# Optimization experiments

Measured on AMD Instinct MI355X. Metric: run time of the kernel, lower is better.

## Reference

```python
import jax, jax.numpy as jnp
import numpy as np

C_IN, C_OUT, K, DG, PAD = 256, 256, 3, 2, 1
EPS = 1e-5


def setup_inputs() -> dict:
    key = jax.random.key(0)
    k = jax.random.split(key, 8)
    B, H, W = 4, 64, 64
    x = jax.random.normal(k[0], (B, C_IN, H, W), jnp.float32)
    # offset/mask conv (DCNv2 pack): 3 * dg * k * k output channels
    w_off = jax.random.normal(k[1], (3 * DG * K * K, C_IN, K, K), jnp.float32) * 0.01
    b_off = jnp.zeros((3 * DG * K * K,), jnp.float32)
    # main deformable conv weight
    w = jax.random.normal(k[2], (C_OUT, C_IN, K, K), jnp.float32) * (1.0 / np.sqrt(C_IN * K * K))
    b = jnp.zeros((C_OUT,), jnp.float32)
    # BatchNorm (eval mode: running stats)
    gamma = jnp.ones((C_OUT,), jnp.float32)
    beta = jnp.zeros((C_OUT,), jnp.float32)
    running_mean = jax.random.normal(k[3], (C_OUT,), jnp.float32) * 0.1
    running_var = jax.random.uniform(k[4], (C_OUT,), jnp.float32, 0.5, 1.5)
    return dict(x=x, w_off=w_off, b_off=b_off, w=w, b=b, gamma=gamma, beta=beta,
                running_mean=running_mean, running_var=running_var)


def _conv2d_same(x, w, b):
    y = jax.lax.conv_general_dilated(x, w, (1, 1), 'SAME',
                                     dimension_numbers=('NCHW', 'OIHW', 'NCHW'))
    return y + b[None, :, None, None]


def _deform_conv(x, w_off, b_off, w, b):
    B, C, H, W = x.shape
    K2 = K * K
    Cg = C // DG
    # offsets + modulation mask from internal conv (DCNv2 pack)
    om = _conv2d_same(x, w_off, b_off)            # [B, 3*DG*K2, H, W]
    o1, o2, m = jnp.split(om, 3, axis=1)
    mask = jax.nn.sigmoid(m).reshape(B, DG, 1, K2, H * W)
    off_y = o1.reshape(B, DG, K2, H, W)
    off_x = o2.reshape(B, DG, K2, H, W)
    # base sampling grid: output pixel + kernel tap - pad
    ki = jnp.arange(K)
    ky = (jnp.repeat(ki, K) - PAD).astype(jnp.float32)   # [K2]
    kx = (jnp.tile(ki, K) - PAD).astype(jnp.float32)     # [K2]
    py = off_y + ky[:, None, None] + jnp.arange(H, dtype=jnp.float32)[None, :, None]
    px = off_x + kx[:, None, None] + jnp.arange(W, dtype=jnp.float32)[None, None, :]
    y0 = jnp.floor(py)
    x0 = jnp.floor(px)
    ly = (py - y0).reshape(B, DG, 1, K2, H * W)
    lx = (px - x0).reshape(B, DG, 1, K2, H * W)
    y0i = y0.astype(jnp.int32)
    x0i = x0.astype(jnp.int32)
    xg = x.reshape(B, DG, Cg, H * W)

    def gather(yi, xi):
        # zero-padded bilinear corner gather, per deformable group
        valid = (yi >= 0) & (yi < H) & (xi >= 0) & (xi < W)
        lin = jnp.clip(yi, 0, H - 1) * W + jnp.clip(xi, 0, W - 1)
        v = jnp.take_along_axis(xg[:, :, :, None, :],
                                lin.reshape(B, DG, 1, K2, H * W), axis=-1)
        return v * valid.reshape(B, DG, 1, K2, H * W)

    val = (gather(y0i, x0i) * (1 - ly) * (1 - lx)
           + gather(y0i, x0i + 1) * (1 - ly) * lx
           + gather(y0i + 1, x0i) * ly * (1 - lx)
           + gather(y0i + 1, x0i + 1) * ly * lx)
    val = val * mask                               # [B, DG, Cg, K2, H*W]
    wr = w.reshape(C_OUT, DG, Cg, K2)
    out = jnp.einsum('bgckn,ogck->bon', val, wr).reshape(B, C_OUT, H, W)
    return out + b[None, :, None, None]


def reference(x, w_off, b_off, w, b, gamma, beta, running_mean, running_var):
    y = _deform_conv(x, w_off, b_off, w, b)
    inv = gamma / jnp.sqrt(running_var + EPS)
    y = (y - running_mean[None, :, None, None]) * inv[None, :, None, None] + beta[None, :, None, None]
    return jax.nn.relu(y)
```

## Files before the change

### kernel.cpp

```cpp
#include <hip/hip_runtime.h>
#include <math.h>

typedef __bf16 bf16x8 __attribute__((ext_vector_type(8)));
typedef float  f32x4  __attribute__((ext_vector_type(4)));
typedef int    i32x4  __attribute__((ext_vector_type(4)));

#define MFMA16(a, b, c) __builtin_amdgcn_mfma_f32_16x16x32_bf16((a), (b), (c), 0, 0, 0)

#define ATIDX(r, c) ((r) * 128 + (((c) ^ ((r) & 7)) * 8))

__global__ __launch_bounds__(256) void setup_kernel(
    const float* __restrict__ x, const float* __restrict__ w,
    const float* __restrict__ w_off, const float* __restrict__ bconv,
    const float* __restrict__ gamma, const float* __restrict__ beta,
    const float* __restrict__ mean, const float* __restrict__ var,
    __bf16* __restrict__ xT, __bf16* __restrict__ wFragD,
    __bf16* __restrict__ wFragO, float* __restrict__ sc,
    float* __restrict__ sh) {
  __shared__ float xs[64][65];
  int t = threadIdx.x;
  if (blockIdx.x < 1024) {
    int b = blockIdx.x >> 8, y = (blockIdx.x >> 2) & 63, cc = blockIdx.x & 3;
    for (int i = t; i < 4096; i += 256) {
      int cl = i >> 6, xc = i & 63;
      xs[cl][xc] = x[(((size_t)b * 256 + cc * 64 + cl) * 64 + y) * 64 + xc];
    }
    __syncthreads();
    for (int i = t; i < 4096; i += 256) {
      int xc = i >> 6, cl = i & 63;
      xT[(((size_t)b * 64 + y) * 64 + xc) * 256 + cc * 64 + cl] = (__bf16)xs[cl][xc];
    }
    return;
  }
  int i = (blockIdx.x - 1024) * 256 + t;
  if (i < 589824) {
    int j = i & 7, lane = (i >> 3) & 63, ocb = (i >> 9) & 15;
    int kc = (i >> 13) & 3, gk = i >> 15;
    int klocal = (lane >> 4) * 8 + j;
    int oc = ocb * 16 + (lane & 15);
    int c = kc * 32 + klocal;
    int g = gk / 9, ktap = gk % 9;
    wFragD[i] = (__bf16)w[((size_t)oc * 256 + g * 128 + c) * 9 + ktap];
  } else {
    int i2 = i - 589824;
    int j = i2 & 7, lane = (i2 >> 3) & 63, ocb = (i2 >> 9) & 3;
    int kc = (i2 >> 11) & 7, tap = i2 >> 14;
    int klocal = (lane >> 4) * 8 + j;
    int oc = ocb * 16 + (lane & 15);
    int ci = kc * 32 + klocal;
    wFragO[i2] = (oc < 54) ? (__bf16)w_off[((size_t)oc * 256 + ci) * 9 + tap]
                           : (__bf16)0.f;
  }
  if (i < 256) {
    float s = gamma[i] * rsqrtf(var[i] + 1e-5f);
    sc[i] = s;
    sh[i] = (bconv[i] - mean[i]) * s + beta[i];
  }
}

struct PhaseC {
  f32x4 swgtv[18 * 64];
  i32x4 slinv[18 * 64];
  __bf16 atile[2][64 * 128];
};
union FusedLDS {
  __bf16 rowbuf[3 * 66 * 256];
  PhaseC c;
};

__global__ __launch_bounds__(1024) void fused_kernel(
    const __bf16* __restrict__ xT, const __bf16* __restrict__ wFragD,
    const __bf16* __restrict__ wFragO, const float* __restrict__ b_off,
    const float* __restrict__ sc, const float* __restrict__ sh,
    float* __restrict__ out) {
  __shared__ __attribute__((aligned(16))) FusedLDS U;
  __shared__ float omrow[54 * 64];
  int t = threadIdx.x;
  int b = blockIdx.x >> 6, y = blockIdx.x & 63;
  int lane = t & 63, wv = t >> 6;
  int l15 = lane & 15, quad = lane >> 4;
  const __bf16* xTb = xT + (size_t)b * 64 * 64 * 256;
  bf16x8 z8;
  #pragma unroll
  for (int e = 0; e < 8; ++e) z8[e] = (__bf16)0.f;

  for (int i = t; i < 3 * 66 * 32; i += 1024) {
    int c = i & 31, px66 = (i >> 5) % 66, dy = i / 2112;
    int y2 = y + dy - 1, x2 = px66 - 1;
    bf16x8 v = z8;
    if (y2 >= 0 && y2 < 64 && x2 >= 0 && x2 < 64)
      v = *(const bf16x8*)(xTb + ((size_t)y2 * 64 + x2) * 256 + c * 8);
    *(bf16x8*)&U.rowbuf[dy * 16896 + px66 * 256 + ((c ^ (px66 & 7)) * 8)] = v;
  }
  __syncthreads();

  if (wv < 4) {
    int ocq = wv;
    f32x4 acc4[4];
    #pragma unroll
    for (int fm = 0; fm < 4; ++fm) acc4[fm] = (f32x4){0.f, 0.f, 0.f, 0.f};
    for (int tap = 0; tap < 9; ++tap) {
      int dy = tap / 3, dxs = tap % 3;
      const __bf16* bb = wFragO + ((size_t)(tap * 8) * 4 + ocq) * 512 + lane * 8;
      const __bf16* rb = U.rowbuf + dy * 16896;
      #pragma unroll
      for (int kc = 0; kc < 8; ++kc) {
        bf16x8 Bf = *(const bf16x8*)(bb + (size_t)kc * 4 * 512);
        int c = kc * 4 + quad;
        #pragma unroll
        for (int fm = 0; fm < 4; ++fm) {
          int p0 = fm * 16 + l15 + dxs;
          bf16x8 a0 = *(const bf16x8*)&rb[p0 * 256 + ((c ^ (p0 & 7)) * 8)];
          acc4[fm] = MFMA16(a0, Bf, acc4[fm]);
        }
      }
    }
    int oc = ocq * 16 + l15;
    if (oc < 54) {
      float bo = b_off[oc];
      #pragma unroll
      for (int fm = 0; fm < 4; ++fm) {
        f32x4 r = {acc4[fm].x + bo, acc4[fm].y + bo,
                   acc4[fm].z + bo, acc4[fm].w + bo};
        *(f32x4*)&omrow[oc * 64 + fm * 16 + quad * 4] = r;
      }
    }
  }
  __syncthreads();

  for (int i = t; i < 18 * 64; i += 1024) {
    int gk = i >> 6, p = i & 63;
    int k = gk % 9;
    float oy = omrow[gk * 64 + p];
    float ox = omrow[(18 + gk) * 64 + p];
    float mz = omrow[(36 + gk) * 64 + p];
    float mv = 1.f / (1.f + expf(-mz));
    float py  = (float)(y + (k / 3) - 1) + oy;
    float pxf = (float)(p + (k % 3) - 1) + ox;
    float y0f = floorf(py), x0f = floorf(pxf);
    int y0 = (int)y0f, x0 = (int)x0f;
    float ly = py - y0f, lx = pxf - x0f;
    int y1 = y0 + 1, x1 = x0 + 1;
    bool vy0 = (y0 >= 0) && (y0 < 64), vy1 = (y1 >= 0) && (y1 < 64);
    bool vx0 = (x0 >= 0) && (x0 < 64), vx1 = (x1 >= 0) && (x1 < 64);
    int cy0 = min(max(y0, 0), 63), cy1 = min(max(y1, 0), 63);
    int cx0 = min(max(x0, 0), 63), cx1 = min(max(x1, 0), 63);
    f32x4 sv;
    sv.x = (vy0 && vx0) ? (1.f - ly) * (1.f - lx) * mv : 0.f;
    sv.y = (vy0 && vx1) ? (1.f - ly) * lx * mv : 0.f;
    sv.z = (vy1 && vx0) ? ly * (1.f - lx) * mv : 0.f;
    sv.w = (vy1 && vx1) ? ly * lx * mv : 0.f;
    i32x4 lv;
    lv.x = (cy0 * 64 + cx0) * 256;
    lv.y = (cy0 * 64 + cx1) * 256;
    lv.z = (cy1 * 64 + cx0) * 256;
    lv.w = (cy1 * 64 + cx1) * 256;
    U.c.swgtv[i] = sv;
    U.c.slinv[i] = lv;
  }
  __syncthreads();

  {
    int p = t >> 4, c16 = t & 15;
    const __bf16* xg = xTb + c16 * 8;
    f32x4 sv = U.c.swgtv[p];
    i32x4 lv = U.c.slinv[p];
    bf16x8 c0 = *(const bf16x8*)(xg + lv.x);
    bf16x8 c1 = *(const bf16x8*)(xg + lv.y);
    bf16x8 c2 = *(const bf16x8*)(xg + lv.z);
    bf16x8 c3 = *(const bf16x8*)(xg + lv.w);
    bf16x8 o;
    #pragma unroll
    for (int e = 0; e < 8; ++e)
      o[e] = (__bf16)(sv.x * (float)c0[e] + sv.y * (float)c1[e]
                    + sv.z * (float)c2[e] + sv.w * (float)c3[e]);
    *(bf16x8*)&U.c.atile[0][ATIDX(p, c16)] = o;
  }

  f32x4 acc[4][2];
  #pragma unroll
  for (int fm = 0; fm < 4; ++fm) {
    acc[fm][0] = (f32x4){0.f, 0.f, 0.f, 0.f};
    acc[fm][1] = (f32x4){0.f, 0.f, 0.f, 0.f};
  }
  int nq = wv - 8;
  bf16x8 bn0, bn1;
  if (wv >= 8) {
    const __bf16* bb = wFragD + ((size_t)nq * 2) * 512 + lane * 8;
    bn0 = *(const bf16x8*)bb;
    bn1 = *(const bf16x8*)(bb + 512);
  }
  __syncthreads();

  for (int gk = 0; gk < 18; ++gk) {
    if (wv < 8) {
      if (gk < 17) {
        int gn = gk + 1;
        int c16 = t & 15, p = t >> 4;
        const __bf16* xg = xTb + (gn / 9) * 128 + c16 * 8;
        __bf16* dst = U.c.atile[(gk + 1) & 1];
        #pragma unroll
        for (int half = 0; half < 2; ++half) {
          int pp = p + half * 32;
          f32x4 sv = U.c.swgtv[gn * 64 + pp];
          i32x4 lv = U.c.slinv[gn * 64 + pp];
          bf16x8 c0 = *(const bf16x8*)(xg + lv.x);
          bf16x8 c1 = *(const bf16x8*)(xg + lv.y);
          bf16x8 c2 = *(const bf16x8*)(xg + lv.z);
          bf16x8 c3 = *(const bf16x8*)(xg + lv.w);
          bf16x8 o;
          #pragma unroll
          for (int e = 0; e < 8; ++e)
            o[e] = (__bf16)(sv.x * (float)c0[e] + sv.y * (float)c1[e]
                          + sv.z * (float)c2[e] + sv.w * (float)c3[e]);
          *(bf16x8*)&dst[ATIDX(pp, c16)] = o;
        }
      }
    } else {
      const __bf16* at = U.c.atile[gk & 1];
      #pragma unroll
      for (int kc = 0; kc < 4; ++kc) {
        bf16x8 b0 = bn0, b1 = bn1;
        int nidx = gk * 4 + kc + 1;
        if (nidx < 72) {
          const __bf16* bb = wFragD + ((size_t)nidx * 16 + nq * 2) * 512 + lane * 8;
          bn0 = *(const bf16x8*)bb;
          bn1 = *(const bf16x8*)(bb + 512);
        }
        #pragma unroll
        for (int fm = 0; fm < 4; ++fm) {
          bf16x8 a = *(const bf16x8*)&at[ATIDX(fm * 16 + l15, kc * 4 + quad)];
          acc[fm][0] = MFMA16(a, b0, acc[fm][0]);
          acc[fm][1] = MFMA16(a, b1, acc[fm][1]);
        }
      }
    }
    __syncthreads();
  }

  if (wv >= 8) {
    #pragma unroll
    for (int fm = 0; fm < 4; ++fm) {
      #pragma unroll
      for (int fn = 0; fn < 2; ++fn) {
        int oc = nq * 32 + fn * 16 + l15;
        float s = sc[oc], h = sh[oc];
        f32x4 v = acc[fm][fn];
        f32x4 r = {fmaxf(v.x * s + h, 0.f), fmaxf(v.y * s + h, 0.f),
                   fmaxf(v.z * s + h, 0.f), fmaxf(v.w * s + h, 0.f)};
        int pxs = fm * 16 + quad * 4;
        *(f32x4*)(out + (((size_t)b * 256 + oc) * 64 + y) * 64 + pxs) = r;
      }
    }
  }
}

extern "C" void kernel_launch(void* const* d_in, const int* in_sizes, int n_in,
                              void* d_out, int out_size, void* d_ws, size_t ws_size,
                              hipStream_t stream) {
  const float* x     = (const float*)d_in[0];
  const float* w_off = (const float*)d_in[1];
  const float* b_off = (const float*)d_in[2];
  const float* w     = (const float*)d_in[3];
  const float* bconv = (const float*)d_in[4];
  const float* gamma = (const float*)d_in[5];
  const float* beta  = (const float*)d_in[6];
  const float* rmean = (const float*)d_in[7];
  const float* rvar  = (const float*)d_in[8];
  float* out = (float*)d_out;

  __bf16* xT     = (__bf16*)d_ws;
  __bf16* wFragD = (__bf16*)((char*)d_ws + 8388608);
  __bf16* wFragO = (__bf16*)((char*)d_ws + 9568256);
  float*  sc     = (float*)((char*)d_ws + 9863168);
  float*  sh     = (float*)((char*)d_ws + 9864192);

  setup_kernel<<<1024 + 2880, 256, 0, stream>>>(
      x, w, w_off, bconv, gamma, beta, rmean, rvar, xT, wFragD, wFragO, sc, sh);
  fused_kernel<<<4 * 64, 1024, 0, stream>>>(xT, wFragD, wFragO, b_off, sc, sh, out);
}
```

Measured before the change: 131.9 us.

## Merge setup and fused kernels into one cooperative kernel with grid sync

Folds the input transpose/bf16 conversion, the weight fragment packing and the BN scale/shift precompute into a single cooperative kernel, using a grid-wide sync before the main deformable conv phase. This removes a kernel launch and the gap between launches. The offset-conv phase no longer stages a 3-row halo buffer in LDS; it reads bf16 input directly from global memory with clamped indices and zero masking. The change relies on all 256 blocks of 1024 threads being co-resident for the grid sync. It also trades cheap LDS reads for repeated global/L2 reads in the offset conv.

```diff
diff --git a/kernel.cpp b/kernel.cpp
--- a/kernel.cpp
+++ b/kernel.cpp
@@ -1,5 +1,8 @@
 #include <hip/hip_runtime.h>
+#include <hip/hip_cooperative_groups.h>
 #include <math.h>
+
+namespace cg = cooperative_groups;
 
 typedef __bf16 bf16x8 __attribute__((ext_vector_type(8)));
 typedef float  f32x4  __attribute__((ext_vector_type(4)));
@@ -8,55 +11,6 @@
 #define MFMA16(a, b, c) __builtin_amdgcn_mfma_f32_16x16x32_bf16((a), (b), (c), 0, 0, 0)
 
 #define ATIDX(r, c) ((r) * 128 + (((c) ^ ((r) & 7)) * 8))
-
-__global__ __launch_bounds__(256) void setup_kernel(
-    const float* __restrict__ x, const float* __restrict__ w,
-    const float* __restrict__ w_off, const float* __restrict__ bconv,
-    const float* __restrict__ gamma, const float* __restrict__ beta,
-    const float* __restrict__ mean, const float* __restrict__ var,
-    __bf16* __restrict__ xT, __bf16* __restrict__ wFragD,
-    __bf16* __restrict__ wFragO, float* __restrict__ sc,
-    float* __restrict__ sh) {
-  __shared__ float xs[64][65];
-  int t = threadIdx.x;
-  if (blockIdx.x < 1024) {
-    int b = blockIdx.x >> 8, y = (blockIdx.x >> 2) & 63, cc = blockIdx.x & 3;
-    for (int i = t; i < 4096; i += 256) {
-      int cl = i >> 6, xc = i & 63;
-      xs[cl][xc] = x[(((size_t)b * 256 + cc * 64 + cl) * 64 + y) * 64 + xc];
-    }
-    __syncthreads();
-    for (int i = t; i < 4096; i += 256) {
-      int xc = i >> 6, cl = i & 63;
-      xT[(((size_t)b * 64 + y) * 64 + xc) * 256 + cc * 64 + cl] = (__bf16)xs[cl][xc];
-    }
-    return;
-  }
-  int i = (blockIdx.x - 1024) * 256 + t;
-  if (i < 589824) {
-    int j = i & 7, lane = (i >> 3) & 63, ocb = (i >> 9) & 15;
-    int kc = (i >> 13) & 3, gk = i >> 15;
-    int klocal = (lane >> 4) * 8 + j;
-    int oc = ocb * 16 + (lane & 15);
-    int c = kc * 32 + klocal;
-    int g = gk / 9, ktap = gk % 9;
-    wFragD[i] = (__bf16)w[((size_t)oc * 256 + g * 128 + c) * 9 + ktap];
-  } else {
-    int i2 = i - 589824;
-    int j = i2 & 7, lane = (i2 >> 3) & 63, ocb = (i2 >> 9) & 3;
-    int kc = (i2 >> 11) & 7, tap = i2 >> 14;
-    int klocal = (lane >> 4) * 8 + j;
-    int oc = ocb * 16 + (lane & 15);
-    int ci = kc * 32 + klocal;
-    wFragO[i2] = (oc < 54) ? (__bf16)w_off[((size_t)oc * 256 + ci) * 9 + tap]
-                           : (__bf16)0.f;
-  }
-  if (i < 256) {
-    float s = gamma[i] * rsqrtf(var[i] + 1e-5f);
-    sc[i] = s;
-    sh[i] = (bconv[i] - mean[i]) * s + beta[i];
-  }
-}
 
 struct PhaseC {
   f32x4 swgtv[18 * 64];
@@ -64,35 +18,75 @@
   __bf16 atile[2][64 * 128];
 };
 union FusedLDS {
-  __bf16 rowbuf[3 * 66 * 256];
+  float xpose[4 * 4160];
   PhaseC c;
 };
 
-__global__ __launch_bounds__(1024) void fused_kernel(
-    const __bf16* __restrict__ xT, const __bf16* __restrict__ wFragD,
-    const __bf16* __restrict__ wFragO, const float* __restrict__ b_off,
-    const float* __restrict__ sc, const float* __restrict__ sh,
-    float* __restrict__ out) {
+__global__ __launch_bounds__(1024) void mega_kernel(
+    const float* __restrict__ x, const float* __restrict__ w,
+    const float* __restrict__ w_off, const float* __restrict__ bconv,
+    const float* __restrict__ gamma, const float* __restrict__ beta,
+    const float* __restrict__ mean, const float* __restrict__ var,
+    const float* __restrict__ b_off, __bf16* __restrict__ xT,
+    __bf16* __restrict__ wFragD, __bf16* __restrict__ wFragO,
+    float* __restrict__ sc, float* __restrict__ sh, float* __restrict__ out) {
   __shared__ __attribute__((aligned(16))) FusedLDS U;
   __shared__ float omrow[54 * 64];
   int t = threadIdx.x;
-  int b = blockIdx.x >> 6, y = blockIdx.x & 63;
+  int bk = blockIdx.x;
   int lane = t & 63, wv = t >> 6;
   int l15 = lane & 15, quad = lane >> 4;
-  const __bf16* xTb = xT + (size_t)b * 64 * 64 * 256;
   bf16x8 z8;
   #pragma unroll
   for (int e = 0; e < 8; ++e) z8[e] = (__bf16)0.f;
 
-  for (int i = t; i < 3 * 66 * 32; i += 1024) {
-    int c = i & 31, px66 = (i >> 5) % 66, dy = i / 2112;
-    int y2 = y + dy - 1, x2 = px66 - 1;
-    bf16x8 v = z8;
-    if (y2 >= 0 && y2 < 64 && x2 >= 0 && x2 < 64)
-      v = *(const bf16x8*)(xTb + ((size_t)y2 * 64 + x2) * 256 + c * 8);
-    *(bf16x8*)&U.rowbuf[dy * 16896 + px66 * 256 + ((c ^ (px66 & 7)) * 8)] = v;
-  }
-  __syncthreads();
+  {
+    int q = t >> 8, tl = t & 255;
+    int u = bk * 4 + q;
+    int ub = u >> 8, uy = (u >> 2) & 63, cc = u & 3;
+    float* xs = U.xpose + q * 4160;
+    for (int i = tl; i < 4096; i += 256) {
+      int cl = i >> 6, xc = i & 63;
+      xs[cl * 65 + xc] = x[(((size_t)ub * 256 + cc * 64 + cl) * 64 + uy) * 64 + xc];
+    }
+    __syncthreads();
+    for (int i = tl; i < 4096; i += 256) {
+      int xc = i >> 6, cl = i & 63;
+      xT[(((size_t)ub * 64 + uy) * 64 + xc) * 256 + cc * 64 + cl] =
+          (__bf16)xs[cl * 65 + xc];
+    }
+  }
+  for (int i = bk * 1024 + t; i < 737280; i += 262144) {
+    if (i < 589824) {
+      int j = i & 7, ln = (i >> 3) & 63, ocb = (i >> 9) & 15;
+      int kc = (i >> 13) & 3, gk = i >> 15;
+      int klocal = (ln >> 4) * 8 + j;
+      int oc = ocb * 16 + (ln & 15);
+      int c = kc * 32 + klocal;
+      int g = gk / 9, ktap = gk % 9;
+      wFragD[i] = (__bf16)w[((size_t)oc * 256 + g * 128 + c) * 9 + ktap];
+    } else {
+      int i2 = i - 589824;
+      int j = i2 & 7, ln = (i2 >> 3) & 63, ocb = (i2 >> 9) & 3;
+      int kc = (i2 >> 11) & 7, tap = i2 >> 14;
+      int klocal = (ln >> 4) * 8 + j;
+      int oc = ocb * 16 + (ln & 15);
+      int ci = kc * 32 + klocal;
+      wFragO[i2] = (oc < 54) ? (__bf16)w_off[((size_t)oc * 256 + ci) * 9 + tap]
+                             : (__bf16)0.f;
+    }
+  }
+  if (bk == 0 && t < 256) {
+    float s = gamma[t] * rsqrtf(var[t] + 1e-5f);
+    sc[t] = s;
+    sh[t] = (bconv[t] - mean[t]) * s + beta[t];
+  }
+
+  __threadfence();
+  cg::this_grid().sync();
+
+  int b = bk >> 6, y = bk & 63;
+  const __bf16* xTb = xT + (size_t)b * 64 * 64 * 256;
 
   if (wv < 4) {
     int ocq = wv;
@@ -101,17 +95,22 @@
     for (int fm = 0; fm < 4; ++fm) acc4[fm] = (f32x4){0.f, 0.f, 0.f, 0.f};
     for (int tap = 0; tap < 9; ++tap) {
       int dy = tap / 3, dxs = tap % 3;
+      int y2 = y + dy - 1;
+      if (y2 < 0 || y2 > 63) continue;
       const __bf16* bb = wFragO + ((size_t)(tap * 8) * 4 + ocq) * 512 + lane * 8;
-      const __bf16* rb = U.rowbuf + dy * 16896;
+      const __bf16* xrow = xTb + (size_t)y2 * 64 * 256 + quad * 8;
+      int px_b = l15 + dxs - 1;
       #pragma unroll
       for (int kc = 0; kc < 8; ++kc) {
         bf16x8 Bf = *(const bf16x8*)(bb + (size_t)kc * 4 * 512);
-        int c = kc * 4 + quad;
         #pragma unroll
         for (int fm = 0; fm < 4; ++fm) {
-          int p0 = fm * 16 + l15 + dxs;
-          bf16x8 a0 = *(const bf16x8*)&rb[p0 * 256 + ((c ^ (p0 & 7)) * 8)];
-          acc4[fm] = MFMA16(a0, Bf, acc4[fm]);
+          int px = px_b + fm * 16;
+          int pxc = min(max(px, 0), 63);
+          bf16x8 av = *(const bf16x8*)(xrow + (size_t)pxc * 256 + kc * 32);
+          bool okx = (px >= 0) && (px < 64);
+          bf16x8 a = okx ? av : z8;
+          acc4[fm] = MFMA16(a, Bf, acc4[fm]);
         }
       }
     }
@@ -275,7 +274,10 @@
   float*  sc     = (float*)((char*)d_ws + 9863168);
   float*  sh     = (float*)((char*)d_ws + 9864192);
 
-  setup_kernel<<<1024 + 2880, 256, 0, stream>>>(
-      x, w, w_off, bconv, gamma, beta, rmean, rvar, xT, wFragD, wFragO, sc, sh);
-  fused_kernel<<<4 * 64, 1024, 0, stream>>>(xT, wFragD, wFragO, b_off, sc, sh, out);
+  void* args[] = {(void*)&x, (void*)&w, (void*)&w_off, (void*)&bconv,
+                  (void*)&gamma, (void*)&beta, (void*)&rmean, (void*)&rvar,
+                  (void*)&b_off, (void*)&xT, (void*)&wFragD, (void*)&wFragO,
+                  (void*)&sc, (void*)&sh, (void*)&out};
+  hipLaunchCooperativeKernel((void*)mega_kernel, dim3(256), dim3(1024),
+                             args, 0, stream);
 }
```

Result: slower. 278.7 us (+111.3%).

## Split each output row across two blocks and drop LDS row staging

Applied to the files above, without the earlier changes.

Each block now handles half an output row (32 pixels), doubling the grid from 256 to 512 blocks so more of the GPU's compute units get work. The offset conv now reads xT directly from global memory with clamped, masked loads instead of staging three padded rows in LDS. Shared memory shrinks and the launch-bounds hint now asks for more occupancy. The tradeoff is that the offset conv and the weight fragments are reloaded by twice as many blocks, and each MFMA wave does half as much work per B-fragment load.

```diff
diff --git a/kernel.cpp b/kernel.cpp
--- a/kernel.cpp
+++ b/kernel.cpp
@@ -58,25 +58,24 @@
   }
 }
 
-struct PhaseC {
-  f32x4 swgtv[18 * 64];
-  i32x4 slinv[18 * 64];
-  __bf16 atile[2][64 * 128];
+struct FusedLDS {
+  f32x4 swgtv[18 * 32];
+  i32x4 slinv[18 * 32];
+  union {
+    float omrow[54 * 32];
+    __bf16 atile[2][32 * 128];
+  } u;
 };
-union FusedLDS {
-  __bf16 rowbuf[3 * 66 * 256];
-  PhaseC c;
-};
-
-__global__ __launch_bounds__(1024) void fused_kernel(
+
+__global__ __launch_bounds__(1024, 8) void fused_kernel(
     const __bf16* __restrict__ xT, const __bf16* __restrict__ wFragD,
     const __bf16* __restrict__ wFragO, const float* __restrict__ b_off,
     const float* __restrict__ sc, const float* __restrict__ sh,
     float* __restrict__ out) {
   __shared__ __attribute__((aligned(16))) FusedLDS U;
-  __shared__ float omrow[54 * 64];
   int t = threadIdx.x;
-  int b = blockIdx.x >> 6, y = blockIdx.x & 63;
+  int bk = blockIdx.x;
+  int b = bk >> 7, y = (bk >> 1) & 63, mh = bk & 1;
   int lane = t & 63, wv = t >> 6;
   int l15 = lane & 15, quad = lane >> 4;
   const __bf16* xTb = xT + (size_t)b * 64 * 64 * 256;
@@ -84,34 +83,28 @@
   #pragma unroll
   for (int e = 0; e < 8; ++e) z8[e] = (__bf16)0.f;
 
-  for (int i = t; i < 3 * 66 * 32; i += 1024) {
-    int c = i & 31, px66 = (i >> 5) % 66, dy = i / 2112;
-    int y2 = y + dy - 1, x2 = px66 - 1;
-    bf16x8 v = z8;
-    if (y2 >= 0 && y2 < 64 && x2 >= 0 && x2 < 64)
-      v = *(const bf16x8*)(xTb + ((size_t)y2 * 64 + x2) * 256 + c * 8);
-    *(bf16x8*)&U.rowbuf[dy * 16896 + px66 * 256 + ((c ^ (px66 & 7)) * 8)] = v;
-  }
-  __syncthreads();
-
   if (wv < 4) {
     int ocq = wv;
-    f32x4 acc4[4];
-    #pragma unroll
-    for (int fm = 0; fm < 4; ++fm) acc4[fm] = (f32x4){0.f, 0.f, 0.f, 0.f};
+    f32x4 acc2[2];
+    acc2[0] = (f32x4){0.f, 0.f, 0.f, 0.f};
+    acc2[1] = (f32x4){0.f, 0.f, 0.f, 0.f};
     for (int tap = 0; tap < 9; ++tap) {
       int dy = tap / 3, dxs = tap % 3;
+      int y2 = y + dy - 1;
+      if (y2 < 0 || y2 > 63) continue;
       const __bf16* bb = wFragO + ((size_t)(tap * 8) * 4 + ocq) * 512 + lane * 8;
-      const __bf16* rb = U.rowbuf + dy * 16896;
+      const __bf16* xrow = xTb + (size_t)y2 * 64 * 256 + quad * 8;
       #pragma unroll
       for (int kc = 0; kc < 8; ++kc) {
         bf16x8 Bf = *(const bf16x8*)(bb + (size_t)kc * 4 * 512);
-        int c = kc * 4 + quad;
         #pragma unroll
-        for (int fm = 0; fm < 4; ++fm) {
-          int p0 = fm * 16 + l15 + dxs;
-          bf16x8 a0 = *(const bf16x8*)&rb[p0 * 256 + ((c ^ (p0 & 7)) * 8)];
-          acc4[fm] = MFMA16(a0, Bf, acc4[fm]);
+        for (int fm = 0; fm < 2; ++fm) {
+          int px = mh * 32 + fm * 16 + l15 + dxs - 1;
+          int pxc = min(max(px, 0), 63);
+          bf16x8 av = *(const bf16x8*)(xrow + (size_t)pxc * 256 + kc * 32);
+          bool okx = (px >= 0) && (px < 64);
+          bf16x8 a = okx ? av : z8;
+          acc2[fm] = MFMA16(a, Bf, acc2[fm]);
         }
       }
     }
@@ -119,21 +112,22 @@
     if (oc < 54) {
       float bo = b_off[oc];
       #pragma unroll
-      for (int fm = 0; fm < 4; ++fm) {
-        f32x4 r = {acc4[fm].x + bo, acc4[fm].y + bo,
-                   acc4[fm].z + bo, acc4[fm].w + bo};
-        *(f32x4*)&omrow[oc * 64 + fm * 16 + quad * 4] = r;
+      for (int fm = 0; fm < 2; ++fm) {
+        f32x4 r = {acc2[fm].x + bo, acc2[fm].y + bo,
+                   acc2[fm].z + bo, acc2[fm].w + bo};
+        *(f32x4*)&U.u.omrow[oc * 32 + fm * 16 + quad * 4] = r;
       }
     }
   }
   __syncthreads();
 
-  for (int i = t; i < 18 * 64; i += 1024) {
-    int gk = i >> 6, p = i & 63;
+  for (int i = t; i < 18 * 32; i += 1024) {
+    int gk = i >> 5, pl = i & 31;
+    int p = mh * 32 + pl;
     int k = gk % 9;
-    float oy = omrow[gk * 64 + p];
-    float ox = omrow[(18 + gk) * 64 + p];
-    float mz = omrow[(36 + gk) * 64 + p];
+    float oy = U.u.omrow[gk * 32 + pl];
+    float ox = U.u.omrow[(18 + gk) * 32 + pl];
+    float mz = U.u.omrow[(36 + gk) * 32 + pl];
     float mv = 1.f / (1.f + expf(-mz));
     float py  = (float)(y + (k / 3) - 1) + oy;
     float pxf = (float)(p + (k % 3) - 1) + ox;
@@ -155,16 +149,16 @@
     lv.y = (cy0 * 64 + cx1) * 256;
     lv.z = (cy1 * 64 + cx0) * 256;
     lv.w = (cy1 * 64 + cx1) * 256;
-    U.c.swgtv[i] = sv;
-    U.c.slinv[i] = lv;
+    U.swgtv[i] = sv;
+    U.slinv[i] = lv;
   }
   __syncthreads();
 
-  {
-    int p = t >> 4, c16 = t & 15;
+  if (t < 512) {
+    int pl = t >> 4, c16 = t & 15;
     const __bf16* xg = xTb + c16 * 8;
-    f32x4 sv = U.c.swgtv[p];
-    i32x4 lv = U.c.slinv[p];
+    f32x4 sv = U.swgtv[pl];
+    i32x4 lv = U.slinv[pl];
     bf16x8 c0 = *(const bf16x8*)(xg + lv.x);
     bf16x8 c1 = *(const bf16x8*)(xg + lv.y);
     bf16x8 c2 = *(const bf16x8*)(xg + lv.z);
@@ -174,12 +168,12 @@
     for (int e = 0; e < 8; ++e)
       o[e] = (__bf16)(sv.x * (float)c0[e] + sv.y * (float)c1[e]
                     + sv.z * (float)c2[e] + sv.w * (float)c3[e]);
-    *(bf16x8*)&U.c.atile[0][ATIDX(p, c16)] = o;
-  }
-
-  f32x4 acc[4][2];
+    *(bf16x8*)&U.u.atile[0][ATIDX(pl, c16)] = o;
+  }
+
+  f32x4 acc[2][2];
   #pragma unroll
-  for (int fm = 0; fm < 4; ++fm) {
+  for (int fm = 0; fm < 2; ++fm) {
     acc[fm][0] = (f32x4){0.f, 0.f, 0.f, 0.f};
     acc[fm][1] = (f32x4){0.f, 0.f, 0.f, 0.f};
   }
@@ -196,28 +190,24 @@
     if (wv < 8) {
       if (gk < 17) {
         int gn = gk + 1;
-        int c16 = t & 15, p = t >> 4;
+        int c16 = t & 15, pl = t >> 4;
         const __bf16* xg = xTb + (gn / 9) * 128 + c16 * 8;
-        __bf16* dst = U.c.atile[(gk + 1) & 1];
+        __bf16* dst = U.u.atile[(gk + 1) & 1];
+        f32x4 sv = U.swgtv[gn * 32 + pl];
+        i32x4 lv = U.slinv[gn * 32 + pl];
+        bf16x8 c0 = *(const bf16x8*)(xg + lv.x);
+        bf16x8 c1 = *(const bf16x8*)(xg + lv.y);
+        bf16x8 c2 = *(const bf16x8*)(xg + lv.z);
+        bf16x8 c3 = *(const bf16x8*)(xg + lv.w);
+        bf16x8 o;
         #pragma unroll
-        for (int half = 0; half < 2; ++half) {
-          int pp = p + half * 32;
-          f32x4 sv = U.c.swgtv[gn * 64 + pp];
-          i32x4 lv = U.c.slinv[gn * 64 + pp];
-          bf16x8 c0 = *(const bf16x8*)(xg + lv.x);
-          bf16x8 c1 = *(const bf16x8*)(xg + lv.y);
-          bf16x8 c2 = *(const bf16x8*)(xg + lv.z);
-          bf16x8 c3 = *(const bf16x8*)(xg + lv.w);
-          bf16x8 o;
-          #pragma unroll
-          for (int e = 0; e < 8; ++e)
-            o[e] = (__bf16)(sv.x * (float)c0[e] + sv.y * (float)c1[e]
-                          + sv.z * (float)c2[e] + sv.w * (float)c3[e]);
-          *(bf16x8*)&dst[ATIDX(pp, c16)] = o;
-        }
+        for (int e = 0; e < 8; ++e)
+          o[e] = (__bf16)(sv.x * (float)c0[e] + sv.y * (float)c1[e]
+                        + sv.z * (float)c2[e] + sv.w * (float)c3[e]);
+        *(bf16x8*)&dst[ATIDX(pl, c16)] = o;
       }
     } else {
-      const __bf16* at = U.c.atile[gk & 1];
+      const __bf16* at = U.u.atile[gk & 1];
       #pragma unroll
       for (int kc = 0; kc < 4; ++kc) {
         bf16x8 b0 = bn0, b1 = bn1;
@@ -228,7 +218,7 @@
           bn1 = *(const bf16x8*)(bb + 512);
         }
         #pragma unroll
-        for (int fm = 0; fm < 4; ++fm) {
+        for (int fm = 0; fm < 2; ++fm) {
           bf16x8 a = *(const bf16x8*)&at[ATIDX(fm * 16 + l15, kc * 4 + quad)];
           acc[fm][0] = MFMA16(a, b0, acc[fm][0]);
           acc[fm][1] = MFMA16(a, b1, acc[fm][1]);
@@ -240,7 +230,7 @@
 
   if (wv >= 8) {
     #pragma unroll
-    for (int fm = 0; fm < 4; ++fm) {
+    for (int fm = 0; fm < 2; ++fm) {
       #pragma unroll
       for (int fn = 0; fn < 2; ++fn) {
         int oc = nq * 32 + fn * 16 + l15;
@@ -248,7 +238,7 @@
         f32x4 v = acc[fm][fn];
         f32x4 r = {fmaxf(v.x * s + h, 0.f), fmaxf(v.y * s + h, 0.f),
                    fmaxf(v.z * s + h, 0.f), fmaxf(v.w * s + h, 0.f)};
-        int pxs = fm * 16 + quad * 4;
+        int pxs = mh * 32 + fm * 16 + quad * 4;
         *(f32x4*)(out + (((size_t)b * 256 + oc) * 64 + y) * 64 + pxs) = r;
       }
     }
@@ -277,5 +267,5 @@
 
   setup_kernel<<<1024 + 2880, 256, 0, stream>>>(
       x, w, w_off, bconv, gamma, beta, rmean, rvar, xT, wFragD, wFragO, sc, sh);
-  fused_kernel<<<4 * 64, 1024, 0, stream>>>(xT, wFragD, wFragO, b_off, sc, sh, out);
+  fused_kernel<<<512, 1024, 0, stream>>>(xT, wFragD, wFragO, b_off, sc, sh, out);
 }
```

Result: slower. 163.9 us (+24.3%).
